# Performance work log

Hardware: AMD Instinct MI355X
Metric: run time of the kernel (lower is better)

The kernel has to match this reference:

```python
import jax, jax.numpy as jnp
import numpy as np
import math

B, S, D, H, F = 4, 1024, 1024, 16, 4096
DH = D // H
NEG = -1000000.0  # matches masked_fill value in MaskedSoftmax
EPS = 1e-5        # torch LayerNorm default


def layer_norm(x, g, b):
    m = jnp.mean(x, axis=-1, keepdims=True)
    v = jnp.mean((x - m) ** 2, axis=-1, keepdims=True)
    return (x - m) * jax.lax.rsqrt(v + EPS) * g + b


def mha(q_in, k_in, v_in, Wq, bq, Wk, bk, Wv, bv, Wo, bo, mask):
    # mask: broadcastable to [B, H, Sq, Sk]; True = keep
    Bq, Sq, _ = q_in.shape
    Sk = k_in.shape[1]
    Q = (q_in @ Wq + bq).reshape(Bq, Sq, H, DH).transpose(0, 2, 1, 3)
    K = (k_in @ Wk + bk).reshape(Bq, Sk, H, DH).transpose(0, 2, 1, 3)
    V = (v_in @ Wv + bv).reshape(Bq, Sk, H, DH).transpose(0, 2, 1, 3)
    scores = jnp.einsum('bhqd,bhkd->bhqk', Q, K) / math.sqrt(DH)
    scores = jnp.where(mask, scores, NEG)
    A = jax.nn.softmax(scores, axis=-1)
    out = jnp.einsum('bhqk,bhkd->bhqd', A, V)
    out = out.transpose(0, 2, 1, 3).reshape(Bq, Sq, D)
    return out @ Wo + bo


def setup_inputs() -> dict:
    key = jax.random.key(0)
    ks = jax.random.split(key, 16)
    w = lambda k, shp: (jax.random.normal(k, shp, dtype=jnp.float32) * 0.02)
    inp = {
        'X': jax.random.normal(ks[0], (B, S, D), dtype=jnp.float32),
        'enc_outputs': jax.random.normal(ks[1], (B, S, D), dtype=jnp.float32),
        'enc_valid_lens': jax.random.randint(ks[2], (B,), 1, S + 1),
        # self-attention
        'Wq1': w(ks[3], (D, D)), 'bq1': jnp.zeros((D,), jnp.float32),
        'Wk1': w(ks[4], (D, D)), 'bk1': jnp.zeros((D,), jnp.float32),
        'Wv1': w(ks[5], (D, D)), 'bv1': jnp.zeros((D,), jnp.float32),
        'Wo1': w(ks[6], (D, D)), 'bo1': jnp.zeros((D,), jnp.float32),
        'g1': jnp.ones((D,), jnp.float32), 'be1': jnp.zeros((D,), jnp.float32),
        # cross-attention
        'Wq2': w(ks[7], (D, D)), 'bq2': jnp.zeros((D,), jnp.float32),
        'Wk2': w(ks[8], (D, D)), 'bk2': jnp.zeros((D,), jnp.float32),
        'Wv2': w(ks[9], (D, D)), 'bv2': jnp.zeros((D,), jnp.float32),
        'Wo2': w(ks[10], (D, D)), 'bo2': jnp.zeros((D,), jnp.float32),
        'g2': jnp.ones((D,), jnp.float32), 'be2': jnp.zeros((D,), jnp.float32),
        # FFN
        'Wf1': w(ks[11], (D, F)), 'bf1': jnp.zeros((F,), jnp.float32),
        'Wf2': w(ks[12], (F, D)), 'bf2': jnp.zeros((D,), jnp.float32),
        'g3': jnp.ones((D,), jnp.float32), 'be3': jnp.zeros((D,), jnp.float32),
    }
    return inp


def reference(X, enc_outputs, enc_valid_lens,
              Wq1, bq1, Wk1, bk1, Wv1, bv1, Wo1, bo1, g1, be1,
              Wq2, bq2, Wk2, bk2, Wv2, bv2, Wo2, bo2, g2, be2,
              Wf1, bf1, Wf2, bf2, g3, be3):
    # training mode, first decode step: key_values = X, causal dec mask
    idx = jnp.arange(S)
    causal = (idx[None, :] <= idx[:, None])[None, None]          # [1,1,S,S]
    cross = (idx[None, :] < enc_valid_lens[:, None])[:, None, None, :]  # [B,1,1,S]

    X2 = mha(X, X, X, Wq1, bq1, Wk1, bk1, Wv1, bv1, Wo1, bo1, causal)
    Y = layer_norm(X2 + X, g1, be1)
    Y2 = mha(Y, enc_outputs, enc_outputs, Wq2, bq2, Wk2, bk2, Wv2, bv2, Wo2, bo2, cross)
    Z = layer_norm(Y2 + Y, g2, be2)
    ffn = jax.nn.relu(Z @ Wf1 + bf1) @ Wf2 + bf2
    return layer_norm(ffn + Z, g3, be3)
```

## Files before the change

### kernel.cpp

```cpp
#include <hip/hip_runtime.h>
#include <stdint.h>

typedef unsigned short u16;
typedef __bf16 bf16x8 __attribute__((ext_vector_type(8)));
typedef float f32x4 __attribute__((ext_vector_type(4)));

#define BB 4
#define SS 1024
#define DD 1024
#define HH 16
#define DHH 64
#define FF 4096
#define NEGV -1000000.0f
#define LOG2E 1.4426950408889634f

__device__ __forceinline__ u16 f2b(float f) {
    uint32_t u = __float_as_uint(f);
    u += 0x7fff + ((u >> 16) & 1);
    return (u16)(u >> 16);
}
__device__ __forceinline__ float b2f(u16 u) {
    return __uint_as_float(((uint32_t)u) << 16);
}

__device__ __forceinline__ float exp2_raw(float x) {
    float r;
    asm volatile("v_exp_f32 %0, %1" : "=v"(r) : "v"(x));
    return r;
}

__device__ __forceinline__ void async16(const void* gp, void* lp) {
    auto g = reinterpret_cast<const __attribute__((address_space(1))) uint32_t*>(
        reinterpret_cast<uintptr_t>(gp));
    auto l = reinterpret_cast<__attribute__((address_space(3))) uint32_t*>(
        reinterpret_cast<uintptr_t>(lp));
    __builtin_amdgcn_global_load_lds(g, l, 16, 0, 0);
}

__global__ void cvt_bf16_kernel(const float* __restrict__ in, u16* __restrict__ out, int n4) {
    int i = blockIdx.x * blockDim.x + threadIdx.x;
    if (i >= n4) return;
    float4 v = reinterpret_cast<const float4*>(in)[i];
    ushort4 o;
    o.x = f2b(v.x); o.y = f2b(v.y); o.z = f2b(v.z); o.w = f2b(v.w);
    reinterpret_cast<ushort4*>(out)[i] = o;
}

__global__ void concat_bias_kernel(const float* __restrict__ a, const float* __restrict__ b,
                                   const float* __restrict__ c, float* __restrict__ out) {
    int i = blockIdx.x * 256 + threadIdx.x;
    float v;
    if (i < 1024) v = a[i];
    else if (i < 2048) v = b[i - 1024];
    else v = c[i - 2048];
    out[i] = v;
}

struct W8 { const float* p[8]; };
__global__ void wtrans8_kernel(W8 wp, u16* __restrict__ dst) {
    __shared__ u16 t[64][68];
    const float* W = wp.p[blockIdx.z];
    u16* Wt = dst + (size_t)blockIdx.z * 1024 * 1024;
    int n0 = blockIdx.x * 64, k0 = blockIdx.y * 64;
    int tx = threadIdx.x & 15, ty = threadIdx.x >> 4;
#pragma unroll
    for (int rr = 0; rr < 4; ++rr) {
        int r = ty + rr * 16;
        float4 v = *reinterpret_cast<const float4*>(&W[(size_t)(k0 + r) * 1024 + n0 + tx * 4]);
        ushort4 o;
        o.x = f2b(v.x); o.y = f2b(v.y); o.z = f2b(v.z); o.w = f2b(v.w);
        *reinterpret_cast<ushort4*>(&t[r][tx * 4]) = o;
    }
    __syncthreads();
#pragma unroll
    for (int rr = 0; rr < 4; ++rr) {
        int n = ty + rr * 16;
        ushort4 o;
        o.x = t[tx * 4 + 0][n];
        o.y = t[tx * 4 + 1][n];
        o.z = t[tx * 4 + 2][n];
        o.w = t[tx * 4 + 3][n];
        *reinterpret_cast<ushort4*>(&Wt[(size_t)(n0 + n) * 1024 + k0 + tx * 4]) = o;
    }
}

__global__ void wtrans_kernel(const float* __restrict__ W, u16* __restrict__ Wt, int K, int N) {
    __shared__ u16 t[64][68];
    int n0 = blockIdx.x * 64, k0 = blockIdx.y * 64;
    int tx = threadIdx.x & 15, ty = threadIdx.x >> 4;
#pragma unroll
    for (int rr = 0; rr < 4; ++rr) {
        int r = ty + rr * 16;
        float4 v = *reinterpret_cast<const float4*>(&W[(size_t)(k0 + r) * N + n0 + tx * 4]);
        ushort4 o;
        o.x = f2b(v.x); o.y = f2b(v.y); o.z = f2b(v.z); o.w = f2b(v.w);
        *reinterpret_cast<ushort4*>(&t[r][tx * 4]) = o;
    }
    __syncthreads();
#pragma unroll
    for (int rr = 0; rr < 4; ++rr) {
        int n = ty + rr * 16;
        ushort4 o;
        o.x = t[tx * 4 + 0][n];
        o.y = t[tx * 4 + 1][n];
        o.z = t[tx * 4 + 2][n];
        o.w = t[tx * 4 + 3][n];
        *reinterpret_cast<ushort4*>(&Wt[(size_t)(n0 + n) * K + k0 + tx * 4]) = o;
    }
}

__global__ void vtrans_kernel(const u16* __restrict__ V, int ldv, u16* __restrict__ VT) {
    __shared__ u16 t[32][33];
    int bh = blockIdx.z;
    int b = bh >> 4, h = bh & 15;
    int s0 = blockIdx.x * 32, d0 = blockIdx.y * 32;
    int tx = threadIdx.x, ty = threadIdx.y;
#pragma unroll
    for (int r = 0; r < 32; r += 8)
        t[ty + r][tx] = V[(size_t)(b * SS + s0 + ty + r) * ldv + h * DHH + d0 + tx];
    __syncthreads();
#pragma unroll
    for (int r = 0; r < 32; r += 8)
        VT[(size_t)(bh * DHH + d0 + ty + r) * SS + s0 + tx] = t[tx][ty + r];
}

template<int BM, bool OUT_BF16, bool RELU, int KSPLIT = 1>
__global__ __launch_bounds__(256, 3) void gemm_bt_kernel(
    const u16* __restrict__ A, const u16* __restrict__ Bt,
    const float* __restrict__ bias, void* __restrict__ Cv,
    int M, int N, int K, int qcols, float qscale)
{
    constexpr int MR = BM / 32;
    __shared__ __attribute__((aligned(16))) u16 As[BM][64];
    __shared__ __attribute__((aligned(16))) u16 Bs[128][64];
    const int tid = threadIdx.x;
    const int lane = tid & 63, wid = tid >> 6;
    const int wr = wid >> 1, wc = wid & 1;
    const int m0 = blockIdx.x * BM, n0 = blockIdx.y * 128;
    const int kz = (KSPLIT > 1) ? blockIdx.z : 0;
    const int Kc = K / KSPLIT;
    const int k0 = kz * Kc;
    const int arow = lane & 15;
    const int kseg = (lane >> 4) * 8;
    const int srow = lane >> 3;
    const int scol = ((lane & 7) ^ srow) * 8;
    const int rswz = (arow & 7) << 3;
    const f32x4 z4 = {0.f, 0.f, 0.f, 0.f};

    f32x4 acc[MR][4];
#pragma unroll
    for (int i = 0; i < MR; ++i)
#pragma unroll
        for (int j = 0; j < 4; ++j) acc[i][j] = z4;

    for (int kt = k0; kt < k0 + Kc; kt += 64) {
        __syncthreads();
#pragma unroll
        for (int i = 0; i < MR; ++i) {
            int ch = wid + i * 4;
            async16(&A[(size_t)(m0 + ch * 8 + srow) * K + kt + scol], &As[ch * 8][0]);
        }
#pragma unroll
        for (int i = 0; i < 4; ++i) {
            int ch = wid + i * 4;
            async16(&Bt[(size_t)(n0 + ch * 8 + srow) * K + kt + scol], &Bs[ch * 8][0]);
        }
        __syncthreads();
#pragma unroll
        for (int ks = 0; ks < 2; ++ks) {
            const int cswz = (ks * 32 + kseg) ^ rswz;
            bf16x8 af[MR], bfr[4];
#pragma unroll
            for (int mi = 0; mi < MR; ++mi)
                af[mi] = *reinterpret_cast<const bf16x8*>(&As[wr * (BM / 2) + mi * 16 + arow][cswz]);
#pragma unroll
            for (int ni = 0; ni < 4; ++ni)
                bfr[ni] = *reinterpret_cast<const bf16x8*>(&Bs[wc * 64 + ni * 16 + arow][cswz]);
#pragma unroll
            for (int mi = 0; mi < MR; ++mi)
#pragma unroll
                for (int ni = 0; ni < 4; ++ni)
                    acc[mi][ni] = __builtin_amdgcn_mfma_f32_16x16x32_bf16(af[mi], bfr[ni], acc[mi][ni], 0, 0, 0);
        }
    }
    const int rrow = (lane >> 4) * 4;
#pragma unroll
    for (int mi = 0; mi < MR; ++mi)
#pragma unroll
        for (int ni = 0; ni < 4; ++ni) {
            int col = n0 + wc * 64 + ni * 16 + arow;
            float bv = (kz == 0) ? bias[col] : 0.f;
            float sc = (col < qcols) ? qscale : 1.f;
#pragma unroll
            for (int r = 0; r < 4; ++r) {
                int row = m0 + wr * (BM / 2) + mi * 16 + rrow + r;
                float v = (acc[mi][ni][r] + bv) * sc;
                if (RELU) v = fmaxf(v, 0.f);
                size_t idx = (size_t)kz * M * N + (size_t)row * N + col;
                if (OUT_BF16) ((u16*)Cv)[idx] = f2b(v);
                else          ((float*)Cv)[idx] = v;
            }
        }
}

__global__ __launch_bounds__(512, 4) void flash_attn_kernel(
    const u16* __restrict__ Q, int ldq, const u16* __restrict__ Kp, int ldk,
    const u16* __restrict__ VT, u16* __restrict__ O,
    const int* __restrict__ vlens, int causal)
{
    __shared__ __attribute__((aligned(16))) u16 Ks[128][64];
    __shared__ __attribute__((aligned(16))) u16 Vs[64][128];
    __shared__ __attribute__((aligned(16))) u16 Ps[128][64];
    const int tid = threadIdx.x, lane = tid & 63, wid = tid >> 6;
    const int bh = blockIdx.x;
    int qb = blockIdx.y;
    if (causal) qb = (bh & 1) ? (7 - qb) : qb;
    const int b = bh >> 4, h = bh & 15;
    const int q0 = qb * 128;
    const int a = lane & 15;
    const int g = lane >> 4;
    const int kseg = g * 8;
    const int srow = lane >> 3;
    const int scol = ((lane & 7) ^ srow) * 8;
    const int vrow = lane >> 4;
    const int rswz = (a & 7) << 3;
    const int vswz = a << 3;
    const f32x4 z4 = {0.f, 0.f, 0.f, 0.f};

    bf16x8 qf[2];
#pragma unroll
    for (int ks = 0; ks < 2; ++ks)
        qf[ks] = *reinterpret_cast<const bf16x8*>(
            &Q[(size_t)(b * SS + q0 + wid * 16 + a) * ldq + h * DHH + ks * 32 + kseg]);

    float m_run = -3e38f, l_run = 0.f;
    f32x4 o[4];
#pragma unroll
    for (int nd = 0; nd < 4; ++nd) o[nd] = z4;

    int vl = causal ? SS : vlens[b];
    int ntiles = causal ? (qb + 1) : ((vl + 127) >> 7);

    for (int kt = 0; kt < ntiles; ++kt) {
        const int kv0 = kt * 128;
        __syncthreads();
#pragma unroll
        for (int i = 0; i < 2; ++i) {
            int ch = wid + i * 8;
            async16(&Kp[(size_t)(b * SS + kv0 + ch * 8 + srow) * ldk + h * DHH + scol], &Ks[ch * 8][0]);
            int cv = wid + i * 8;
            int vs = (cv * 4 + vrow) & 15;
            async16(&VT[(size_t)(bh * DHH + cv * 4 + vrow) * SS + kv0 + ((lane & 15) ^ vs) * 8], &Vs[cv * 4][0]);
        }
        __syncthreads();

        f32x4 st[8];
#pragma unroll
        for (int ni = 0; ni < 8; ++ni) st[ni] = z4;
        __builtin_amdgcn_s_setprio(1);
#pragma unroll
        for (int ks = 0; ks < 2; ++ks) {
            const int cswz = (ks * 32 + kseg) ^ rswz;
            bf16x8 kf[8];
#pragma unroll
            for (int ni = 0; ni < 8; ++ni)
                kf[ni] = *reinterpret_cast<const bf16x8*>(&Ks[ni * 16 + a][cswz]);
#pragma unroll
            for (int ni = 0; ni < 8; ++ni)
                st[ni] = __builtin_amdgcn_mfma_f32_16x16x32_bf16(kf[ni], qf[ks], st[ni], 0, 0, 0);
        }
        __builtin_amdgcn_s_setprio(0);

        bool domask = causal ? (kt == qb) : (kv0 + 128 > vl);
        if (domask) {
            const int qg = q0 + wid * 16 + a;
#pragma unroll
            for (int ni = 0; ni < 8; ++ni)
#pragma unroll
                for (int r = 0; r < 4; ++r) {
                    int cg = kv0 + ni * 16 + 4 * g + r;
                    bool keep = causal ? (cg <= qg) : (cg < vl);
                    if (!keep) st[ni][r] = NEGV;
                }
        }

        float tm = -3e38f;
#pragma unroll
        for (int ni = 0; ni < 8; ++ni)
#pragma unroll
            for (int r = 0; r < 4; ++r) tm = fmaxf(tm, st[ni][r]);
        tm = fmaxf(tm, __shfl_xor(tm, 16));
        tm = fmaxf(tm, __shfl_xor(tm, 32));
        bool need = __any(tm > m_run + 11.0f);
        float corr = 1.f;
        if (need) {
            float nm = fmaxf(m_run, tm);
            corr = exp2_raw(m_run - nm);
            m_run = nm;
        }
        float rs = 0.f;
#pragma unroll
        for (int ni = 0; ni < 8; ++ni)
#pragma unroll
            for (int r = 0; r < 4; ++r) {
                float p = exp2_raw(st[ni][r] - m_run);
                st[ni][r] = p;
                rs += p;
            }
        rs += __shfl_xor(rs, 16);
        rs += __shfl_xor(rs, 32);
        l_run = l_run * corr + rs;

        if (need) {
#pragma unroll
            for (int r = 0; r < 4; ++r) {
                float cr = __shfl(corr, (lane & 48) + 4 * g + r);
#pragma unroll
                for (int nd = 0; nd < 4; ++nd) o[nd][r] *= cr;
            }
        }

#pragma unroll
        for (int hh = 0; hh < 2; ++hh) {
#pragma unroll
            for (int ni4 = 0; ni4 < 4; ++ni4) {
                int ni = hh * 4 + ni4;
                uint2 pw;
                pw.x = (uint32_t)f2b(st[ni][0]) | ((uint32_t)f2b(st[ni][1]) << 16);
                pw.y = (uint32_t)f2b(st[ni][2]) | ((uint32_t)f2b(st[ni][3]) << 16);
                int prow = wid * 16 + a;
                int pcol = (ni4 * 16 + 4 * g) ^ rswz;
                *reinterpret_cast<uint2*>(&Ps[prow][pcol]) = pw;
            }
            __builtin_amdgcn_s_setprio(1);
#pragma unroll
            for (int kk = 0; kk < 2; ++kk) {
                const int kf_ = hh * 2 + kk;
                const int pswz = (kk * 32 + kseg) ^ rswz;
                const int cvswz = (kf_ * 32 + kseg) ^ vswz;
                bf16x8 pa, vb[4];
                pa = *reinterpret_cast<const bf16x8*>(&Ps[wid * 16 + a][pswz]);
#pragma unroll
                for (int nd = 0; nd < 4; ++nd)
                    vb[nd] = *reinterpret_cast<const bf16x8*>(&Vs[nd * 16 + a][cvswz]);
#pragma unroll
                for (int nd = 0; nd < 4; ++nd)
                    o[nd] = __builtin_amdgcn_mfma_f32_16x16x32_bf16(pa, vb[nd], o[nd], 0, 0, 0);
            }
            __builtin_amdgcn_s_setprio(0);
        }
    }

    float il = 1.f / l_run;
#pragma unroll
    for (int r = 0; r < 4; ++r) {
        float ilr = __shfl(il, (lane & 48) + 4 * g + r);
        int row = q0 + wid * 16 + 4 * g + r;
#pragma unroll
        for (int nd = 0; nd < 4; ++nd)
            O[(size_t)(b * SS + row) * DD + h * DHH + nd * 16 + a] = f2b(o[nd][r] * ilr);
    }
}

__global__ void add_ln_kernel(const u16* __restrict__ A, const u16* __restrict__ A2,
                              const float* __restrict__ R,
                              const float* __restrict__ g, const float* __restrict__ be,
                              float* __restrict__ out32, u16* __restrict__ out16)
{
    __shared__ float red[4][2];
    const int row = blockIdx.x, tid = threadIdx.x;
    const size_t base = (size_t)row * DD;
    ushort4 ua = *reinterpret_cast<const ushort4*>(A + base + tid * 4);
    ushort4 ub = *reinterpret_cast<const ushort4*>(A2 + base + tid * 4);
    float4 vr = *reinterpret_cast<const float4*>(R + base + tid * 4);
    float x0 = b2f(ua.x) + b2f(ub.x) + vr.x, x1 = b2f(ua.y) + b2f(ub.y) + vr.y;
    float x2 = b2f(ua.z) + b2f(ub.z) + vr.z, x3 = b2f(ua.w) + b2f(ub.w) + vr.w;
    float s = x0 + x1 + x2 + x3;
    float q = x0 * x0 + x1 * x1 + x2 * x2 + x3 * x3;
#pragma unroll
    for (int off = 32; off; off >>= 1) {
        s += __shfl_xor(s, off);
        q += __shfl_xor(q, off);
    }
    if ((tid & 63) == 0) { red[tid >> 6][0] = s; red[tid >> 6][1] = q; }
    __syncthreads();
    s = red[0][0] + red[1][0] + red[2][0] + red[3][0];
    q = red[0][1] + red[1][1] + red[2][1] + red[3][1];
    float mean = s * (1.f / 1024.f);
    float var = q * (1.f / 1024.f) - mean * mean;
    float rstd = rsqrtf(var + 1e-5f);
    int c = tid * 4;
    float o0 = (x0 - mean) * rstd * g[c + 0] + be[c + 0];
    float o1 = (x1 - mean) * rstd * g[c + 1] + be[c + 1];
    float o2 = (x2 - mean) * rstd * g[c + 2] + be[c + 2];
    float o3 = (x3 - mean) * rstd * g[c + 3] + be[c + 3];
    float4 ov = {o0, o1, o2, o3};
    *reinterpret_cast<float4*>(out32 + base + c) = ov;
    if (out16) {
        ushort4 hv;
        hv.x = f2b(o0); hv.y = f2b(o1); hv.z = f2b(o2); hv.w = f2b(o3);
        *reinterpret_cast<ushort4*>(out16 + base + c) = hv;
    }
}

extern "C" void kernel_launch(void* const* d_in, const int* in_sizes, int n_in,
                              void* d_out, int out_size, void* d_ws, size_t ws_size,
                              hipStream_t stream)
{
    const float* X   = (const float*)d_in[0];
    const float* ENC = (const float*)d_in[1];
    const int*   VL  = (const int*)d_in[2];
    const float* Wq1 = (const float*)d_in[3];  const float* bq1 = (const float*)d_in[4];
    const float* Wk1 = (const float*)d_in[5];  const float* bk1 = (const float*)d_in[6];
    const float* Wv1 = (const float*)d_in[7];  const float* bv1 = (const float*)d_in[8];
    const float* Wo1 = (const float*)d_in[9];  const float* bo1 = (const float*)d_in[10];
    const float* g1  = (const float*)d_in[11]; const float* be1 = (const float*)d_in[12];
    const float* Wq2 = (const float*)d_in[13]; const float* bq2 = (const float*)d_in[14];
    const float* Wk2 = (const float*)d_in[15]; const float* bk2 = (const float*)d_in[16];
    const float* Wv2 = (const float*)d_in[17]; const float* bv2 = (const float*)d_in[18];
    const float* Wo2 = (const float*)d_in[19]; const float* bo2 = (const float*)d_in[20];
    const float* g2  = (const float*)d_in[21]; const float* be2 = (const float*)d_in[22];
    const float* Wf1 = (const float*)d_in[23]; const float* bf1 = (const float*)d_in[24];
    const float* Wf2 = (const float*)d_in[25]; const float* bf2 = (const float*)d_in[26];
    const float* g3  = (const float*)d_in[27]; const float* be3 = (const float*)d_in[28];

    char* ws = (char*)d_ws;
    const size_t MB = 1024 * 1024;
    u16*   XBF  = (u16*)(ws + 0 * MB);
    u16*   ENCB = (u16*)(ws + 8 * MB);
    u16*   WTsq = (u16*)(ws + 16 * MB);
    u16*   WTf1 = (u16*)(ws + 32 * MB);
    u16*   WTf2 = (u16*)(ws + 40 * MB);
    u16*   QKV  = (u16*)(ws + 48 * MB);
    u16*   HF   = (u16*)(ws + 48 * MB);
    u16*   VTb  = (u16*)(ws + 80 * MB);
    u16*   AO   = (u16*)(ws + 88 * MB);
    u16*   P16  = (u16*)(ws + 96 * MB);
    float* Y32  = (float*)(ws + 112 * MB);
    u16*   YBF  = (u16*)(ws + 128 * MB);
    float* Z32  = (float*)(ws + 136 * MB);
    u16*   ZBF  = (u16*)(ws + 152 * MB);
    float* B1 = (float*)d_out;
    float* B2 = (float*)d_out + 4096;
    (void)ws_size; (void)in_sizes; (void)n_in; (void)out_size;

    const int M = BB * SS;
    const size_t MN = (size_t)M * DD;
    const float QS = 0.125f * LOG2E;

    cvt_bf16_kernel<<<M * DD / 4 / 256, 256, 0, stream>>>(X, XBF, M * DD / 4);
    cvt_bf16_kernel<<<M * DD / 4 / 256, 256, 0, stream>>>(ENC, ENCB, M * DD / 4);
    concat_bias_kernel<<<12, 256, 0, stream>>>(bq1, bk1, bv1, B1);
    concat_bias_kernel<<<8, 256, 0, stream>>>(bk2, bv2, bv2, B2);
    W8 w8 = {{Wq1, Wk1, Wv1, Wo1, Wq2, Wk2, Wv2, Wo2}};
    wtrans8_kernel<<<dim3(16, 16, 8), 256, 0, stream>>>(w8, WTsq);
    wtrans_kernel<<<dim3(64, 16), 256, 0, stream>>>(Wf1, WTf1, DD, FF);
    wtrans_kernel<<<dim3(16, 64), 256, 0, stream>>>(Wf2, WTf2, FF, DD);

    gemm_bt_kernel<128, true, false><<<dim3(32, 24), 256, 0, stream>>>(XBF, WTsq, B1, QKV, M, 3072, DD, 1024, QS);
    vtrans_kernel<<<dim3(32, 2, 64), dim3(32, 8), 0, stream>>>(QKV + 2048, 3072, VTb);
    flash_attn_kernel<<<dim3(64, 8), 512, 0, stream>>>(QKV, 3072, QKV + 1024, 3072, VTb, AO, VL, 1);
    gemm_bt_kernel<128, true, false, 2><<<dim3(32, 8, 2), 256, 0, stream>>>(AO, WTsq + 3u * 1024 * 1024, bo1, P16, M, DD, DD, 0, 1.f);
    add_ln_kernel<<<M, 256, 0, stream>>>(P16, P16 + MN, X, g1, be1, Y32, YBF);

    gemm_bt_kernel<64, true, false><<<dim3(64, 8), 256, 0, stream>>>(YBF, WTsq + 4u * 1024 * 1024, bq2, XBF, M, DD, DD, 1024, QS);
    gemm_bt_kernel<128, true, false><<<dim3(32, 16), 256, 0, stream>>>(ENCB, WTsq + 5u * 1024 * 1024, B2, QKV, M, 2048, DD, 0, 1.f);
    vtrans_kernel<<<dim3(32, 2, 64), dim3(32, 8), 0, stream>>>(QKV + 1024, 2048, VTb);
    flash_attn_kernel<<<dim3(64, 8), 512, 0, stream>>>(XBF, 1024, QKV, 2048, VTb, AO, VL, 0);
    gemm_bt_kernel<128, true, false, 2><<<dim3(32, 8, 2), 256, 0, stream>>>(AO, WTsq + 7u * 1024 * 1024, bo2, P16, M, DD, DD, 0, 1.f);
    add_ln_kernel<<<M, 256, 0, stream>>>(P16, P16 + MN, Y32, g2, be2, Z32, ZBF);

    gemm_bt_kernel<128, true, true><<<dim3(32, 32), 256, 0, stream>>>(ZBF, WTf1, bf1, HF, M, FF, DD, 0, 1.f);
    gemm_bt_kernel<128, true, false, 2><<<dim3(32, 8, 2), 256, 0, stream>>>(HF, WTf2, bf2, P16, M, DD, FF, 0, 1.f);
    add_ln_kernel<<<M, 256, 0, stream>>>(P16, P16 + MN, Z32, g3, be3, (float*)d_out, nullptr);
}
```

Before: 326.5 us.

## Add 256x256 tiled GEMM kernel for QKV and FFN matmuls with split-K partials

Introduces a 512-thread GEMM with 256x256 output tiles, double-buffered async LDS staging with XOR swizzle and interleaved prefetch, used for the fused QKV projection and both FFN GEMMs. The second FFN GEMM uses 4-way split-K, so add_ln is templated to sum a variable number of bf16 partial buffers. Larger tiles raise arithmetic intensity and cut global reloads, but they mean fewer workgroups (192-256) on a 256-CU part and higher register pressure. Split-K also adds partial-sum write and read traffic.

After: 316.7 us. -3.0%, faster.

```diff
diff --git a/kernel.cpp b/kernel.cpp
--- a/kernel.cpp
+++ b/kernel.cpp
@@ -22,13 +22,11 @@
 __device__ __forceinline__ float b2f(u16 u) {
     return __uint_as_float(((uint32_t)u) << 16);
 }
-
 __device__ __forceinline__ float exp2_raw(float x) {
     float r;
     asm volatile("v_exp_f32 %0, %1" : "=v"(r) : "v"(x));
     return r;
 }
-
 __device__ __forceinline__ void async16(const void* gp, void* lp) {
     auto g = reinterpret_cast<const __attribute__((address_space(1))) uint32_t*>(
         reinterpret_cast<uintptr_t>(gp));
@@ -194,6 +192,123 @@
 #pragma unroll
             for (int r = 0; r < 4; ++r) {
                 int row = m0 + wr * (BM / 2) + mi * 16 + rrow + r;
+                float v = (acc[mi][ni][r] + bv) * sc;
+                if (RELU) v = fmaxf(v, 0.f);
+                size_t idx = (size_t)kz * M * N + (size_t)row * N + col;
+                if (OUT_BF16) ((u16*)Cv)[idx] = f2b(v);
+                else          ((float*)Cv)[idx] = v;
+            }
+        }
+}
+
+template<bool OUT_BF16, bool RELU, int KSPLIT = 1>
+__global__ __launch_bounds__(512, 2) void gemm256_kernel(
+    const u16* __restrict__ A, const u16* __restrict__ Bt,
+    const float* __restrict__ bias, void* __restrict__ Cv,
+    int M, int N, int K, int qcols, float qscale)
+{
+    __shared__ __attribute__((aligned(16))) u16 As[2][256][64];
+    __shared__ __attribute__((aligned(16))) u16 Bs[2][256][64];
+    const int tid = threadIdx.x, lane = tid & 63, wid = tid >> 6;
+    const int wr = wid >> 2, wc = wid & 3;
+    const int gx = gridDim.x, nwg = gridDim.x * gridDim.y;
+    int bid = blockIdx.y * gx + blockIdx.x;
+    int swz = (bid & 7) * (nwg >> 3) + (bid >> 3);
+    const int m0 = (swz % gx) * 256, n0 = (swz / gx) * 256;
+    const int kz = (KSPLIT > 1) ? blockIdx.z : 0;
+    const int Kc = K / KSPLIT, k0 = kz * Kc, NT = Kc >> 6;
+    const int a = lane & 15, g = lane >> 4;
+    const int srow = lane >> 3;
+    const int scol = ((lane & 7) ^ srow) * 8;
+    const int rswz = (a & 7) << 3;
+    const f32x4 z4 = {0.f, 0.f, 0.f, 0.f};
+
+    f32x4 acc[8][4];
+#pragma unroll
+    for (int i = 0; i < 8; ++i)
+#pragma unroll
+        for (int j = 0; j < 4; ++j) acc[i][j] = z4;
+
+    auto stageA = [&](int t, int h) {
+        int kt = k0 + t * 64;
+#pragma unroll
+        for (int i = 0; i < 2; ++i) {
+            int row = h * 128 + (wid * 2 + i) * 8;
+            async16(&A[(size_t)(m0 + row + srow) * K + kt + scol], &As[t & 1][row][0]);
+        }
+    };
+    auto stageB = [&](int t, int h) {
+        int kt = k0 + t * 64;
+#pragma unroll
+        for (int i = 0; i < 2; ++i) {
+            int row = h * 128 + (wid * 2 + i) * 8;
+            async16(&Bt[(size_t)(n0 + row + srow) * K + kt + scol], &Bs[t & 1][row][0]);
+        }
+    };
+
+    stageA(0, 0); stageA(0, 1); stageB(0, 0); stageB(0, 1);
+    stageA(1, 0); stageA(1, 1); stageB(1, 0); stageB(1, 1);
+    asm volatile("s_waitcnt vmcnt(8)" ::: "memory");
+    __builtin_amdgcn_s_barrier();
+    asm volatile("" ::: "memory");
+
+    for (int t = 0; t < NT; ++t) {
+        const int b = t & 1;
+        bf16x8 bf[4][2];
+#pragma unroll
+        for (int p = 0; p < 4; ++p) {
+            bf16x8 af[2][2];
+#pragma unroll
+            for (int m2 = 0; m2 < 2; ++m2)
+#pragma unroll
+                for (int ks = 0; ks < 2; ++ks)
+                    af[m2][ks] = *reinterpret_cast<const bf16x8*>(
+                        &As[b][wr * 128 + (p * 2 + m2) * 16 + a][(ks * 32 + g * 8) ^ rswz]);
+            if (p == 0) {
+#pragma unroll
+                for (int ni = 0; ni < 4; ++ni)
+#pragma unroll
+                    for (int ks = 0; ks < 2; ++ks)
+                        bf[ni][ks] = *reinterpret_cast<const bf16x8*>(
+                            &Bs[b][wc * 64 + ni * 16 + a][(ks * 32 + g * 8) ^ rswz]);
+            }
+            if (p == 0 && t >= 1 && t + 1 < NT) stageA(t + 1, 0);
+            if (p == 1 && t >= 1 && t + 1 < NT) stageA(t + 1, 1);
+            if (p == 2 && t + 2 < NT) stageB(t + 2, 0);
+            if (p == 3 && t + 2 < NT) stageB(t + 2, 1);
+            asm volatile("" ::: "memory");
+            __builtin_amdgcn_s_barrier();
+            asm volatile("" ::: "memory");
+            __builtin_amdgcn_s_setprio(1);
+#pragma unroll
+            for (int ks = 0; ks < 2; ++ks)
+#pragma unroll
+                for (int m2 = 0; m2 < 2; ++m2)
+#pragma unroll
+                    for (int ni = 0; ni < 4; ++ni)
+                        acc[p * 2 + m2][ni] = __builtin_amdgcn_mfma_f32_16x16x32_bf16(
+                            af[m2][ks], bf[ni][ks], acc[p * 2 + m2][ni], 0, 0, 0);
+            __builtin_amdgcn_s_setprio(0);
+        }
+        if (t < NT - 1) {
+            if (t < NT - 2) asm volatile("s_waitcnt vmcnt(4)" ::: "memory");
+            else            asm volatile("s_waitcnt vmcnt(0)" ::: "memory");
+            __builtin_amdgcn_s_barrier();
+            asm volatile("" ::: "memory");
+        }
+    }
+
+    const int rrow = g * 4;
+#pragma unroll
+    for (int mi = 0; mi < 8; ++mi)
+#pragma unroll
+        for (int ni = 0; ni < 4; ++ni) {
+            int col = n0 + wc * 64 + ni * 16 + a;
+            float bv = (kz == 0) ? bias[col] : 0.f;
+            float sc = (col < qcols) ? qscale : 1.f;
+#pragma unroll
+            for (int r = 0; r < 4; ++r) {
+                int row = m0 + wr * 128 + mi * 16 + rrow + r;
                 float v = (acc[mi][ni][r] + bv) * sc;
                 if (RELU) v = fmaxf(v, 0.f);
                 size_t idx = (size_t)kz * M * N + (size_t)row * N + col;
@@ -362,7 +477,8 @@
     }
 }
 
-__global__ void add_ln_kernel(const u16* __restrict__ A, const u16* __restrict__ A2,
+template<int NP>
+__global__ void add_ln_kernel(const u16* __restrict__ P, size_t pstride,
                               const float* __restrict__ R,
                               const float* __restrict__ g, const float* __restrict__ be,
                               float* __restrict__ out32, u16* __restrict__ out16)
@@ -370,11 +486,13 @@
     __shared__ float red[4][2];
     const int row = blockIdx.x, tid = threadIdx.x;
     const size_t base = (size_t)row * DD;
-    ushort4 ua = *reinterpret_cast<const ushort4*>(A + base + tid * 4);
-    ushort4 ub = *reinterpret_cast<const ushort4*>(A2 + base + tid * 4);
     float4 vr = *reinterpret_cast<const float4*>(R + base + tid * 4);
-    float x0 = b2f(ua.x) + b2f(ub.x) + vr.x, x1 = b2f(ua.y) + b2f(ub.y) + vr.y;
-    float x2 = b2f(ua.z) + b2f(ub.z) + vr.z, x3 = b2f(ua.w) + b2f(ub.w) + vr.w;
+    float x0 = vr.x, x1 = vr.y, x2 = vr.z, x3 = vr.w;
+#pragma unroll
+    for (int p = 0; p < NP; ++p) {
+        ushort4 u = *reinterpret_cast<const ushort4*>(P + p * pstride + base + tid * 4);
+        x0 += b2f(u.x); x1 += b2f(u.y); x2 += b2f(u.z); x3 += b2f(u.w);
+    }
     float s = x0 + x1 + x2 + x3;
     float q = x0 * x0 + x1 * x1 + x2 * x2 + x3 * x3;
 #pragma unroll
@@ -435,6 +553,7 @@
     u16*   HF   = (u16*)(ws + 48 * MB);
     u16*   VTb  = (u16*)(ws + 80 * MB);
     u16*   AO   = (u16*)(ws + 88 * MB);
+    u16*   P4   = (u16*)(ws + 80 * MB);
     u16*   P16  = (u16*)(ws + 96 * MB);
     float* Y32  = (float*)(ws + 112 * MB);
     u16*   YBF  = (u16*)(ws + 128 * MB);
@@ -457,20 +576,20 @@
     wtrans_kernel<<<dim3(64, 16), 256, 0, stream>>>(Wf1, WTf1, DD, FF);
     wtrans_kernel<<<dim3(16, 64), 256, 0, stream>>>(Wf2, WTf2, FF, DD);
 
-    gemm_bt_kernel<128, true, false><<<dim3(32, 24), 256, 0, stream>>>(XBF, WTsq, B1, QKV, M, 3072, DD, 1024, QS);
+    gemm256_kernel<true, false><<<dim3(16, 12), 512, 0, stream>>>(XBF, WTsq, B1, QKV, M, 3072, DD, 1024, QS);
     vtrans_kernel<<<dim3(32, 2, 64), dim3(32, 8), 0, stream>>>(QKV + 2048, 3072, VTb);
     flash_attn_kernel<<<dim3(64, 8), 512, 0, stream>>>(QKV, 3072, QKV + 1024, 3072, VTb, AO, VL, 1);
     gemm_bt_kernel<128, true, false, 2><<<dim3(32, 8, 2), 256, 0, stream>>>(AO, WTsq + 3u * 1024 * 1024, bo1, P16, M, DD, DD, 0, 1.f);
-    add_ln_kernel<<<M, 256, 0, stream>>>(P16, P16 + MN, X, g1, be1, Y32, YBF);
+    add_ln_kernel<2><<<M, 256, 0, stream>>>(P16, MN, X, g1, be1, Y32, YBF);
 
     gemm_bt_kernel<64, true, false><<<dim3(64, 8), 256, 0, stream>>>(YBF, WTsq + 4u * 1024 * 1024, bq2, XBF, M, DD, DD, 1024, QS);
     gemm_bt_kernel<128, true, false><<<dim3(32, 16), 256, 0, stream>>>(ENCB, WTsq + 5u * 1024 * 1024, B2, QKV, M, 2048, DD, 0, 1.f);
     vtrans_kernel<<<dim3(32, 2, 64), dim3(32, 8), 0, stream>>>(QKV + 1024, 2048, VTb);
     flash_attn_kernel<<<dim3(64, 8), 512, 0, stream>>>(XBF, 1024, QKV, 2048, VTb, AO, VL, 0);
     gemm_bt_kernel<128, true, false, 2><<<dim3(32, 8, 2), 256, 0, stream>>>(AO, WTsq + 7u * 1024 * 1024, bo2, P16, M, DD, DD, 0, 1.f);
-    add_ln_kernel<<<M, 256, 0, stream>>>(P16, P16 + MN, Y32, g2, be2, Z32, ZBF);
-
-    gemm_bt_kernel<128, true, true><<<dim3(32, 32), 256, 0, stream>>>(ZBF, WTf1, bf1, HF, M, FF, DD, 0, 1.f);
-    gemm_bt_kernel<128, true, false, 2><<<dim3(32, 8, 2), 256, 0, stream>>>(HF, WTf2, bf2, P16, M, DD, FF, 0, 1.f);
-    add_ln_kernel<<<M, 256, 0, stream>>>(P16, P16 + MN, Z32, g3, be3, (float*)d_out, nullptr);
-}
+    add_ln_kernel<2><<<M, 256, 0, stream>>>(P16, MN, Y32, g2, be2, Z32, ZBF);
+
+    gemm256_kernel<true, true><<<dim3(16, 16), 512, 0, stream>>>(ZBF, WTf1, bf1, HF, M, FF, DD, 0, 1.f);
+    gemm256_kernel<true, false, 4><<<dim3(16, 4, 4), 512, 0, stream>>>(HF, WTf2, bf2, P4, M, DD, FF, 0, 1.f);
+    add_ln_kernel<4><<<M, 256, 0, stream>>>(P4, MN, Z32, g3, be3, (float*)d_out, nullptr);
+}
```
